# Kernel optimization log

Measured on AMD Instinct MI355X. Metric: run time of the kernel, lower is better.

Reference implementation:

```python
import jax, jax.numpy as jnp
import numpy as np

NUM_STARTS = 64  # num_continuous_samples: candidate window start positions


def setup_inputs():
    key = jax.random.key(0)
    k1, k2, k3 = jax.random.split(key, 3)
    T, B, C, M, K = 128, 8, 6, 32, 16
    times = jnp.arange(T, dtype=jnp.float32)
    path = jax.random.normal(k1, (B, T, C), dtype=jnp.float32)
    # lengths initialised uniform in [max_shapelet_length/2, max_shapelet_length] = [20, 40]
    lengths = jax.random.uniform(k2, (M,), minval=20.0, maxval=40.0, dtype=jnp.float32)
    shapelets = jax.random.uniform(k3, (M, K, C), minval=-1.0, maxval=1.0, dtype=jnp.float32)
    return {"times": times, "path": path, "lengths": lengths, "shapelets": shapelets}


def _forward(times, path, lengths, shapelets):
    T = times.shape[0]
    M, K, C = shapelets.shape
    S = NUM_STARTS
    t0, tN = times[0], times[-1]
    # candidate start positions of each shapelet's window: (M, S)
    frac = jnp.linspace(0.0, 1.0, S)
    starts = t0 + frac[None, :] * (tN - t0 - lengths[:, None])
    ends = starts + lengths[:, None]
    # shapelet knot times (shapelet is piecewise linear on a uniform grid over its length): (M, S, K)
    kfrac = jnp.linspace(0.0, 1.0, K)
    shp_knots = starts[..., None] + lengths[:, None, None] * kfrac
    # union knot set: path knots + shapelet knots, clamped to the window.
    # knots outside the window collapse onto the window edge -> zero-width intervals -> zero contribution.
    path_knots = jnp.broadcast_to(times, (M, S, T))
    ts = jnp.sort(jnp.concatenate([path_knots, shp_knots], axis=-1), axis=-1)  # (M, S, P)
    ts = jnp.clip(ts, starts[..., None], ends[..., None])
    # evaluate the continuous piecewise-linear path at ts: (B, M, S, P, C)
    idx = jnp.clip(jnp.searchsorted(times, ts, side='right') - 1, 0, T - 2)
    w = ((ts - times[idx]) / (times[idx + 1] - times[idx]))[None, ..., None]
    path_vals = path[:, idx, :] * (1.0 - w) + path[:, idx + 1, :] * w
    # evaluate the continuous piecewise-linear shapelet at ts: (M, S, P, C)
    h = lengths / (K - 1)  # knot spacing per shapelet
    rel = (ts - starts[..., None]) / h[:, None, None]
    sidx = jnp.clip(jnp.floor(rel).astype(jnp.int32), 0, K - 2)
    sw = (rel - sidx)[..., None]
    m_ix = jnp.arange(M)[:, None, None]
    shp_vals = shapelets[m_ix, sidx] * (1.0 - sw) + shapelets[m_ix, sidx + 1] * sw
    # exact L2 discrepancy between the two piecewise-linear functions:
    # on each interval diff is linear, int_0^1 ||(1-u)da + u db||^2 du = (|da|^2 + da.db + |db|^2)/3
    d = path_vals - shp_vals[None]                       # (B, M, S, P, C)
    dt = ts[..., 1:] - ts[..., :-1]                      # (M, S, P-1)
    da, db = d[..., :-1, :], d[..., 1:, :]
    quad = (jnp.sum(da * da, -1) + jnp.sum(da * db, -1) + jnp.sum(db * db, -1)) / 3.0
    disc = jnp.sqrt(jnp.sum(dt[None] * quad, axis=-1))   # (B, M, S)
    # sliding-window minimum over start positions
    return jnp.min(disc, axis=-1)                        # (B, M)


def reference(times, path, lengths, shapelets):
    return _forward(times, path, lengths, shapelets)
```

## Files before the change

### kernel.cpp

```cpp
#include <hip/hip_runtime.h>


__global__ __launch_bounds__(256) void shapelet_kernel(
    const float* __restrict__ path,
    const float* __restrict__ lengths,
    const float* __restrict__ shapelets,
    float* __restrict__ out)
{
    const int bm  = (int)blockIdx.x;
    const int m   = bm & 31;
    const int b   = bm >> 5;
    const int tid = (int)threadIdx.x;

    __shared__ float pl[768];
    __shared__ float shp[96];
    __shared__ float red[4];

    if (tid < 192) {
        ((float4*)pl)[tid] = ((const float4*)(path + b * 768))[tid];
    } else if (tid < 216) {
        ((float4*)shp)[tid - 192] = ((const float4*)(shapelets + m * 96))[tid - 192];
    }
    const float len = lengths[m];
    __syncthreads();

    const int s = tid >> 2;
    const int q = tid & 3;

    const float start = ((float)s * (1.0f / 63.0f)) * (127.0f - len);
    const float kstep = len * (1.0f / 15.0f);
    const float inv_h = 15.0f / len;

    const int k0 = 4 * q;
    const int k1 = (q == 3) ? 15 : (k0 + 4);

    float tprev = start + (float)k0 * kstep;

    float dprev[6], dcur[6];
    {
        const float t = tprev;
        int idx = (int)t; if (idx > 126) idx = 126;
        const float w = t - (float)idx;
        const float rel = (t - start) * inv_h;
        int si = (int)rel; if (si > 14) si = 14;
        const float sw = rel - (float)si;
        const float* p  = pl  + idx * 6;
        const float* sp = shp + si  * 6;
        #pragma unroll
        for (int c = 0; c < 6; ++c) {
            const float pv = p[c]  + w  * (p[c + 6]  - p[c]);
            const float sv = sp[c] + sw * (sp[c + 6] - sp[c]);
            dprev[c] = pv - sv;
        }
    }

    float acc = 0.0f;
    int i = (int)tprev + 1;

    for (int k = k0 + 1; k <= k1; ++k) {
        const float tk = start + (float)k * kstep;
        for (;;) {
            const float ti = (float)i;
            const bool is_int = (ti < tk);
            const float t = is_int ? ti : tk;

            int idx = (int)t; if (idx > 126) idx = 126;
            const float w = t - (float)idx;
            const float rel = (t - start) * inv_h;
            int si = (int)rel; if (si > 14) si = 14;
            const float sw = rel - (float)si;
            const float* p  = pl  + idx * 6;
            const float* sp = shp + si  * 6;

            float qsum = 0.0f;
            #pragma unroll
            for (int c = 0; c < 6; ++c) {
                const float pv = p[c]  + w  * (p[c + 6]  - p[c]);
                const float sv = sp[c] + sw * (sp[c + 6] - sp[c]);
                const float d  = pv - sv;
                qsum += dprev[c] * dprev[c] + dprev[c] * d + d * d;
                dcur[c] = d;
            }
            acc += (t - tprev) * (qsum * (1.0f / 3.0f));
            tprev = t;
            #pragma unroll
            for (int c = 0; c < 6; ++c) dprev[c] = dcur[c];

            if (is_int) { ++i; } else { break; }
        }
    }

    float v = acc;
    v += __shfl_xor(v, 1, 64);
    v += __shfl_xor(v, 2, 64);
    float disc = sqrtf(v);

    disc = fminf(disc, __shfl_xor(disc, 4, 64));
    disc = fminf(disc, __shfl_xor(disc, 8, 64));
    disc = fminf(disc, __shfl_xor(disc, 16, 64));
    disc = fminf(disc, __shfl_xor(disc, 32, 64));

    if ((tid & 63) == 0) red[tid >> 6] = disc;
    __syncthreads();
    if (tid == 0) {
        out[bm] = fminf(fminf(red[0], red[1]), fminf(red[2], red[3]));
    }
}

extern "C" void kernel_launch(void* const* d_in, const int* in_sizes, int n_in,
                              void* d_out, int out_size, void* d_ws, size_t ws_size,
                              hipStream_t stream)
{
    const float* path      = (const float*)d_in[1];
    const float* lengths   = (const float*)d_in[2];
    const float* shapelets = (const float*)d_in[3];
    float* out = (float*)d_out;

    shapelet_kernel<<<dim3(256), dim3(256), 0, stream>>>(path, lengths, shapelets, out);
}
```

Before: 63.55 us.

## Split each window into one thread per shapelet segment, 1024-thread blocks

Each start position is now handled by 16 threads, 15 of which each integrate a single shapelet segment, instead of 4 threads covering several segments each. This shortens the serial per-thread loop and lets the shapelet endpoints of a segment be hoisted into registers, removing the per-step shapelet index computation and its LDS loads. Path rows are read as float2 vectors. The cost is 1024-thread blocks with one idle lane in every 16, a longer shuffle reduction, and a 16-entry cross-wave min.

```diff
diff --git a/kernel.cpp b/kernel.cpp
--- a/kernel.cpp
+++ b/kernel.cpp
@@ -1,7 +1,7 @@
 #include <hip/hip_runtime.h>
 
 
-__global__ __launch_bounds__(256) void shapelet_kernel(
+__global__ __launch_bounds__(1024) void shapelet_kernel(
     const float* __restrict__ path,
     const float* __restrict__ lengths,
     const float* __restrict__ shapelets,
@@ -14,7 +14,7 @@
 
     __shared__ float pl[768];
     __shared__ float shp[96];
-    __shared__ float red[4];
+    __shared__ float red[16];
 
     if (tid < 192) {
         ((float4*)pl)[tid] = ((const float4*)(path + b * 768))[tid];
@@ -24,86 +24,90 @@
     const float len = lengths[m];
     __syncthreads();
 
-    const int s = tid >> 2;
-    const int q = tid & 3;
+    const int s   = tid >> 4;
+    const int seg = tid & 15;
 
     const float start = ((float)s * (1.0f / 63.0f)) * (127.0f - len);
     const float kstep = len * (1.0f / 15.0f);
     const float inv_h = 15.0f / len;
 
-    const int k0 = 4 * q;
-    const int k1 = (q == 3) ? 15 : (k0 + 4);
+    float acc = 0.0f;
 
-    float tprev = start + (float)k0 * kstep;
+    if (seg < 15) {
+        const float tL = start + (float)seg * kstep;
+        const float tR = start + (float)(seg + 1) * kstep;
 
-    float dprev[6], dcur[6];
-    {
-        const float t = tprev;
-        int idx = (int)t; if (idx > 126) idx = 126;
-        const float w = t - (float)idx;
-        const float rel = (t - start) * inv_h;
-        int si = (int)rel; if (si > 14) si = 14;
-        const float sw = rel - (float)si;
-        const float* p  = pl  + idx * 6;
-        const float* sp = shp + si  * 6;
-        #pragma unroll
-        for (int c = 0; c < 6; ++c) {
-            const float pv = p[c]  + w  * (p[c + 6]  - p[c]);
-            const float sv = sp[c] + sw * (sp[c + 6] - sp[c]);
-            dprev[c] = pv - sv;
+        float s0[6], sd[6];
+        {
+            const float2* q2 = (const float2*)(shp + seg * 6);
+            const float2 a0 = q2[0], a1 = q2[1], a2 = q2[2];
+            const float2 b0 = q2[3], b1 = q2[4], b2 = q2[5];
+            s0[0] = a0.x; s0[1] = a0.y; s0[2] = a1.x;
+            s0[3] = a1.y; s0[4] = a2.x; s0[5] = a2.y;
+            sd[0] = b0.x - s0[0]; sd[1] = b0.y - s0[1]; sd[2] = b1.x - s0[2];
+            sd[3] = b1.y - s0[3]; sd[4] = b2.x - s0[4]; sd[5] = b2.y - s0[5];
         }
-    }
 
-    float acc = 0.0f;
-    int i = (int)tprev + 1;
+        float dprev[6];
+        auto eval = [&](float t, float* d) {
+            int idx = (int)t; if (idx > 126) idx = 126;
+            const float w  = t - (float)idx;
+            const float sw = (t - start) * inv_h - (float)seg;
+            const float2* p2 = (const float2*)(pl + idx * 6);
+            const float2 r0 = p2[0], r1 = p2[1], r2 = p2[2];
+            const float2 r3 = p2[3], r4 = p2[4], r5 = p2[5];
+            const float pa[6] = { r0.x, r0.y, r1.x, r1.y, r2.x, r2.y };
+            const float pb[6] = { r3.x, r3.y, r4.x, r4.y, r5.x, r5.y };
+            #pragma unroll
+            for (int c = 0; c < 6; ++c) {
+                const float pv = pa[c] + w * (pb[c] - pa[c]);
+                const float sv = s0[c] + sw * sd[c];
+                d[c] = pv - sv;
+            }
+        };
 
-    for (int k = k0 + 1; k <= k1; ++k) {
-        const float tk = start + (float)k * kstep;
+        eval(tL, dprev);
+        float tprev = tL;
+
+        int i = (int)tL + 1;
         for (;;) {
             const float ti = (float)i;
-            const bool is_int = (ti < tk);
-            const float t = is_int ? ti : tk;
+            const bool is_int = (ti < tR);
+            const float t = is_int ? ti : tR;
 
-            int idx = (int)t; if (idx > 126) idx = 126;
-            const float w = t - (float)idx;
-            const float rel = (t - start) * inv_h;
-            int si = (int)rel; if (si > 14) si = 14;
-            const float sw = rel - (float)si;
-            const float* p  = pl  + idx * 6;
-            const float* sp = shp + si  * 6;
-
+            float d[6];
+            eval(t, d);
             float qsum = 0.0f;
             #pragma unroll
             for (int c = 0; c < 6; ++c) {
-                const float pv = p[c]  + w  * (p[c + 6]  - p[c]);
-                const float sv = sp[c] + sw * (sp[c + 6] - sp[c]);
-                const float d  = pv - sv;
-                qsum += dprev[c] * dprev[c] + dprev[c] * d + d * d;
-                dcur[c] = d;
+                qsum += dprev[c] * dprev[c] + dprev[c] * d[c] + d[c] * d[c];
+                dprev[c] = d[c];
             }
             acc += (t - tprev) * (qsum * (1.0f / 3.0f));
             tprev = t;
-            #pragma unroll
-            for (int c = 0; c < 6; ++c) dprev[c] = dcur[c];
 
-            if (is_int) { ++i; } else { break; }
+            if (!is_int) break;
+            ++i;
         }
     }
 
     float v = acc;
     v += __shfl_xor(v, 1, 64);
     v += __shfl_xor(v, 2, 64);
+    v += __shfl_xor(v, 4, 64);
+    v += __shfl_xor(v, 8, 64);
     float disc = sqrtf(v);
 
-    disc = fminf(disc, __shfl_xor(disc, 4, 64));
-    disc = fminf(disc, __shfl_xor(disc, 8, 64));
     disc = fminf(disc, __shfl_xor(disc, 16, 64));
     disc = fminf(disc, __shfl_xor(disc, 32, 64));
 
     if ((tid & 63) == 0) red[tid >> 6] = disc;
     __syncthreads();
     if (tid == 0) {
-        out[bm] = fminf(fminf(red[0], red[1]), fminf(red[2], red[3]));
+        float r = red[0];
+        #pragma unroll
+        for (int wv = 1; wv < 16; ++wv) r = fminf(r, red[wv]);
+        out[bm] = r;
     }
 }
 
@@ -116,5 +120,5 @@
     const float* shapelets = (const float*)d_in[3];
     float* out = (float*)d_out;
 
-    shapelet_kernel<<<dim3(256), dim3(256), 0, stream>>>(path, lengths, shapelets, out);
+    shapelet_kernel<<<dim3(256), dim3(1024), 0, stream>>>(path, lengths, shapelets, out);
 }
```

Result: faster. 62.27 us (-2.0%).
